# Kernel optimization log

Hardware: AMD Instinct MI355X
Metric: run time of the kernel (lower is better)

## Reference

```python
import jax, jax.numpy as jnp
import numpy as np

B, S, H, A = 64, 200, 256, 16
CAPS_LAYERS = 3
NEG = -1e9
LN_EPS = 1e-12


def _layernorm(x, g, b):
    mu = jnp.mean(x, axis=-1, keepdims=True)
    var = jnp.mean(jnp.square(x - mu), axis=-1, keepdims=True)
    return (x - mu) / jnp.sqrt(var + LN_EPS) * g + b


def setup_inputs() -> dict:
    key = jax.random.key(0)
    ks = jax.random.split(key, 10)
    s = 0.02  # initializer_range
    return {
        "item_emb": jax.random.normal(ks[0], (B, S, H), jnp.float32),
        "item_seq": jax.random.randint(ks[1], (B, S), 0, 50000),
        "time_seq": jax.random.randint(ks[2], (B, S, 2), 0, 14),
        "W_lin": s * jax.random.normal(ks[3], (H, H), jnp.float32),
        "b_lin": jnp.zeros((H,), jnp.float32),
        "aspect_embs": s * jax.random.normal(ks[4], (A, H), jnp.float32),
        "pos_emb": s * jax.random.normal(ks[5], (S, H), jnp.float32),
        "tdt_emb": s * jax.random.normal(ks[6], (14, H), jnp.float32),
        "tdn_emb": s * jax.random.normal(ks[7], (14, H), jnp.float32),
        "Wa1": s * jax.random.normal(ks[8], (H, H), jnp.float32),
        "ba1": jnp.zeros((H,), jnp.float32),
        "Wa2": s * jax.random.normal(ks[9], (H,), jnp.float32),
        "ba2": jnp.zeros((1,), jnp.float32),
        "ln_g": jnp.ones((H,), jnp.float32),
        "ln_b": jnp.zeros((H,), jnp.float32),
    }


def reference(item_emb, item_seq, time_seq, W_lin, b_lin, aspect_embs,
              pos_emb, tdt_emb, tdn_emb, Wa1, ba1, Wa2, ba2, ln_g, ln_b):
    b, s = item_emb.shape[0], item_emb.shape[1]
    pad = item_seq == 0  # [B,S]

    # ---- TimeAwareAttention (seq_output has a singleton neighbor dim in torch) ----
    td = tdt_emb[time_seq[:, :, 0]] + tdn_emb[time_seq[:, :, 1]]       # [B,S,H]
    tma_in = pos_emb[None, :s] + item_emb + td                          # [B,S,H]
    h = tma_in @ Wa1 + ba1
    h = jnp.where(h >= 0, h, 0.01 * h)                                  # LeakyReLU
    w = h @ Wa2 + ba2[0]                                                # [B,S]
    w = jnp.where(pad, NEG, w)
    tma = jax.nn.softmax(w, axis=-1)                                    # [B,S]

    # ---- gating (eval: clean gates) ----
    gates = jnp.einsum('bsh,ah->bsa', item_emb, aspect_embs)            # [B,S,A]
    idx = jnp.argmax(gates, axis=-1)                                    # topk k=1, [B,S]

    src = jnp.where(pad, 0.0, 1.0)
    counts = jnp.zeros((b, A), jnp.float32).at[jnp.arange(b)[:, None], idx].add(src)
    aspect_mask = counts == 0                                           # [B,A]

    # ---- item transform (dropout = identity in eval) ----
    moe = _layernorm(jnp.tanh(item_emb @ W_lin + b_lin) + item_emb, ln_g, ln_b)  # [B,S,H]

    # ---- capsule routing ----
    bij = gates
    cap = jnp.broadcast_to(aspect_embs[None], (b, A, H))
    for _ in range(CAPS_LAYERS):
        cij = jnp.where(aspect_mask[:, None, :], NEG, bij)
        cij = jax.nn.softmax(cij, axis=-1)
        cij = jnp.where(pad[:, :, None], 0.0, cij)                      # [B,S,A]
        cap = jnp.einsum('bsa,bsh,bs->bah', cij, moe, tma)              # [B,A,H]
        n2 = jnp.sum(jnp.square(cap), axis=-1, keepdims=True)
        cap = n2 / (1.0 + n2) / jnp.sqrt(n2 + 1e-9) * cap               # squash
        bij = bij + jnp.einsum('bsh,bah->bsa', moe, cap)

    # ---- gather activated interests / activation positions ----
    activated = cap[jnp.arange(b)[:, None], idx]                        # [B,S,H]
    seq_pos = jnp.where(pad, 0, jnp.arange(1, s + 1)[None, :]).astype(jnp.float32)
    act_mat = jnp.full((b, s, A), -1.0, jnp.float32)
    act_mat = act_mat.at[jnp.arange(b)[:, None], jnp.arange(s)[None, :], idx].set(seq_pos)
    act_mat = jnp.where(pad[:, :, None], -1.0, act_mat)
    max_pos = jnp.max(act_mat, axis=1)                                  # [B,A]
    aspects_item_idx = jnp.where(max_pos > -1.0, max_pos - 1.0, max_pos)

    gates_sm = jax.nn.softmax(gates, axis=-1)
    return (cap, gates_sm, aspect_mask, activated, aspects_item_idx, idx[:, :, None])
```

## Files before the change

kernel.cpp:

```cpp
#include <hip/hip_runtime.h>

#define B_ 64
#define S_ 200
#define H_ 256
#define A_ 16
#define M_ (B_*S_)
#define NEGV (-1000000000.0f)

typedef unsigned short ushortT;
typedef __attribute__((ext_vector_type(8))) short short8;
typedef __attribute__((ext_vector_type(4))) float f32x4;

__device__ __forceinline__ ushortT bf16u(float f) {
  unsigned int u = __builtin_bit_cast(unsigned int, f);
  unsigned int r = (u + 0x7fffu + ((u >> 16) & 1u)) >> 16;
  return (ushortT)r;
}
__device__ __forceinline__ float bf2f(ushortT u) {
  unsigned int v = ((unsigned int)u) << 16;
  return __builtin_bit_cast(float, v);
}

__global__ __launch_bounds__(256) void prep_kernel(
    const float* __restrict__ item, const int* __restrict__ iseq,
    const int* __restrict__ tseq, const float* __restrict__ Wa1,
    const float* __restrict__ W_lin, const float* __restrict__ asp,
    const float* __restrict__ pos, const float* __restrict__ tdt,
    const float* __restrict__ tdn,
    ushortT* __restrict__ itemB, ushortT* __restrict__ tmaB,
    ushortT* __restrict__ Wa1T, ushortT* __restrict__ WlinT,
    float* __restrict__ gates_raw, float* __restrict__ idxf)
{
  const int blk = blockIdx.x;
  const int t = threadIdx.x;

  if (blk >= 800) {
    __shared__ float T[64*65];
    int wsel = (blk - 800) >> 4;
    int tile = (blk - 800) & 15;
    const float* W = wsel ? W_lin : Wa1;
    ushortT* WT = wsel ? WlinT : Wa1T;
    int tr = (tile >> 2) * 64, tc = (tile & 3) * 64;
    #pragma unroll
    for (int p = 0; p < 16; ++p) {
      int r = p*4 + (t >> 6);
      int c = t & 63;
      T[c*65 + r] = W[(tr + r)*H_ + tc + c];
    }
    __syncthreads();
    #pragma unroll
    for (int p = 0; p < 16; ++p) {
      int n = p*4 + (t >> 6);
      int k = t & 63;
      WT[(tc + n)*H_ + tr + k] = bf16u(T[n*65 + k]);
    }
    return;
  }

  __shared__ float aspl[16*260];
  __shared__ float gL[16*20];
  __shared__ int sL[16], ttL[16], tnL[16];

  const int m0 = blk * 16;
  if (t < 16) {
    int m = m0 + t;
    sL[t]  = m % S_;
    ttL[t] = tseq[2*m];
    tnL[t] = tseq[2*m+1];
  }
  #pragma unroll
  for (int i = 0; i < 4; ++i) {
    int e = t + 256*i;
    int r = e >> 6, c = e & 63;
    *(float4*)&aspl[r*260 + 4*c] = *(const float4*)&asp[r*H_ + 4*c];
  }
  __syncthreads();

  #pragma unroll 4
  for (int r = 0; r < 16; ++r) {
    int m = m0 + r;
    float iv = item[(size_t)m*H_ + t];
    float tv = iv + pos[sL[r]*H_ + t] + tdt[ttL[r]*H_ + t] + tdn[tnL[r]*H_ + t];
    itemB[(size_t)m*H_ + t] = bf16u(iv);
    tmaB[(size_t)m*H_ + t]  = bf16u(tv);
  }

  {
    int r = t >> 4, a = t & 15;
    int m = m0 + r;
    float g = 0.f;
    #pragma unroll 4
    for (int k4 = 0; k4 < 64; ++k4) {
      float4 xv = *(const float4*)&item[(size_t)m*H_ + 4*k4];
      float4 av = *(const float4*)&aspl[a*260 + 4*k4];
      g += xv.x*av.x + xv.y*av.y + xv.z*av.z + xv.w*av.w;
    }
    gL[r*20 + a] = g;
  }
  __syncthreads();
  if (t < 64) {
    int r = t >> 2, q = t & 3;
    float4 gv;
    gv.x = gL[r*20 + 4*q + 0]; gv.y = gL[r*20 + 4*q + 1];
    gv.z = gL[r*20 + 4*q + 2]; gv.w = gL[r*20 + 4*q + 3];
    *(float4*)&gates_raw[(m0+r)*A_ + 4*q] = gv;
  }
  if (t < 16) {
    float best = gL[t*20]; int bi = 0;
    #pragma unroll
    for (int a = 1; a < 16; ++a) {
      float v = gL[t*20 + a];
      if (v > best) { best = v; bi = a; }
    }
    idxf[m0 + t] = (float)bi;
  }
}

__global__ __launch_bounds__(256) void gemm_kernel(
    const ushortT* __restrict__ tmaB, const ushortT* __restrict__ itemB,
    const ushortT* __restrict__ Wa1T, const ushortT* __restrict__ WlinT,
    const float* __restrict__ item, const int* __restrict__ iseq,
    const float* __restrict__ ba1, const float* __restrict__ Wa2,
    const float* __restrict__ ba2, const float* __restrict__ b_lin,
    const float* __restrict__ g_ln, const float* __restrict__ b_ln,
    float* __restrict__ w_out, ushortT* __restrict__ moe_outB)
{
  __shared__ ushortT Al[64*40];
  __shared__ ushortT Bl[256*40];

  const int g = blockIdx.y;
  const ushortT* __restrict__ Ap  = g ? itemB : tmaB;
  const ushortT* __restrict__ WTp = g ? WlinT : Wa1T;

  const int t = threadIdx.x;
  const int m0 = blockIdx.x * 64;
  const int lane = t & 63, w = t >> 6;
  const int col = lane & 15;
  const int rg  = lane >> 4;

  f32x4 acc[16];
  #pragma unroll
  for (int i = 0; i < 16; ++i) acc[i] = (f32x4){0.f,0.f,0.f,0.f};

  const int ar = t >> 2, akq = (t & 3) * 8;

  for (int k0 = 0; k0 < H_; k0 += 32) {
    __syncthreads();
    *(uint4*)&Al[ar*40 + akq] = *(const uint4*)&Ap[(size_t)(m0 + ar)*H_ + k0 + akq];
    #pragma unroll
    for (int i = 0; i < 4; ++i) {
      int n = i*64 + ar;
      *(uint4*)&Bl[n*40 + akq] = *(const uint4*)&WTp[(size_t)n*H_ + k0 + akq];
    }
    __syncthreads();
    short8 af = *(const short8*)&Al[(w*16 + col)*40 + rg*8];
    #pragma unroll
    for (int q = 0; q < 16; ++q) {
      short8 bf = *(const short8*)&Bl[(q*16 + col)*40 + rg*8];
      acc[q] = __builtin_amdgcn_mfma_f32_16x16x32_bf16(af, bf, acc[q], 0, 0, 0);
    }
  }

  if (g == 0) {
    float bav[16], wav[16];
    #pragma unroll
    for (int q = 0; q < 16; ++q) {
      int n = q*16 + col;
      bav[q] = ba1[n]; wav[q] = Wa2[n];
    }
    float bb2 = ba2[0];
    #pragma unroll
    for (int j = 0; j < 4; ++j) {
      float p = 0.f;
      #pragma unroll
      for (int q = 0; q < 16; ++q) {
        float h = acc[q][j] + bav[q];
        h = (h >= 0.f) ? h : 0.01f*h;
        p += h * wav[q];
      }
      #pragma unroll
      for (int mk = 1; mk < 16; mk <<= 1) p += __shfl_xor(p, mk);
      if (col == 0) {
        int m = m0 + w*16 + rg*4 + j;
        w_out[m] = (iseq[m] == 0) ? NEGV : (p + bb2);
      }
    }
  } else {
    float blv[16], glv[16], bbv[16];
    #pragma unroll
    for (int q = 0; q < 16; ++q) {
      int n = q*16 + col;
      blv[q] = b_lin[n]; glv[q] = g_ln[n]; bbv[q] = b_ln[n];
    }
    #pragma unroll
    for (int j = 0; j < 4; ++j) {
      int m = m0 + w*16 + rg*4 + j;
      float v[16];
      float s1 = 0.f, s2 = 0.f;
      #pragma unroll
      for (int q = 0; q < 16; ++q) {
        float iv = item[(size_t)m*H_ + q*16 + col];
        float vv = tanhf(acc[q][j] + blv[q]) + iv;
        v[q] = vv; s1 += vv; s2 += vv*vv;
      }
      #pragma unroll
      for (int mk = 1; mk < 16; mk <<= 1) {
        s1 += __shfl_xor(s1, mk);
        s2 += __shfl_xor(s2, mk);
      }
      float mu  = s1 * (1.0f/H_);
      float var = s2 * (1.0f/H_) - mu*mu;
      float rs  = 1.0f / sqrtf(fmaxf(var, 0.f) + 1e-12f);
      #pragma unroll
      for (int q = 0; q < 16; ++q)
        moe_outB[(size_t)m*H_ + q*16 + col] = bf16u((v[q] - mu)*rs*glv[q] + bbv[q]);
    }
  }
}

__device__ __forceinline__ float blk_max(float v, float* red) {
  #pragma unroll
  for (int mk = 32; mk; mk >>= 1) v = fmaxf(v, __shfl_xor(v, mk));
  int t = threadIdx.x;
  if ((t & 63) == 0) red[t >> 6] = v;
  __syncthreads();
  if (t < 64) {
    float x = (t < 16) ? red[t] : -3.0e38f;
    #pragma unroll
    for (int mk = 8; mk; mk >>= 1) x = fmaxf(x, __shfl_xor(x, mk));
    if (t == 0) red[0] = x;
  }
  __syncthreads();
  float r = red[0];
  __syncthreads();
  return r;
}

__device__ __forceinline__ float blk_sum(float v, float* red) {
  #pragma unroll
  for (int mk = 32; mk; mk >>= 1) v += __shfl_xor(v, mk);
  int t = threadIdx.x;
  if ((t & 63) == 0) red[t >> 6] = v;
  __syncthreads();
  if (t < 64) {
    float x = (t < 16) ? red[t] : 0.f;
    #pragma unroll
    for (int mk = 8; mk; mk >>= 1) x += __shfl_xor(x, mk);
    if (t == 0) red[0] = x;
  }
  __syncthreads();
  float r = red[0];
  __syncthreads();
  return r;
}

#define WGSTR 232
#define CBSTR 260
#define CLSTR 252

__global__ __launch_bounds__(1024) void phaseC_kernel(
    const int* __restrict__ iseq, const float* __restrict__ w_in,
    const ushortT* __restrict__ moeB, const float* __restrict__ idxf,
    float* __restrict__ gates_rs,
    float* __restrict__ cap_out,
    float* __restrict__ mask_out,
    float* __restrict__ aidx_out,
    float* __restrict__ act_out)
{
  __shared__ ushortT moeTr[57344];
  __shared__ ushortT wgtT[16*WGSTR];
  __shared__ ushortT capB[16*CBSTR];
  __shared__ float bij[4032];
  __shared__ float n2p[16*17];
  __shared__ float n2s[16];
  __shared__ float tmaL[S_];
  __shared__ float red[16];
  __shared__ float maskf[A_];
  __shared__ int counts[A_], maxpos[A_];
  __shared__ int idxl[S_];
  __shared__ int padl[S_];

  const int t = threadIdx.x;
  const int b = blockIdx.x;
  const int base = b * S_;
  const int lane = t & 63, w = t >> 6;
  const int la = lane & 15, lg = lane >> 4;

  #pragma unroll
  for (int u = 0; u < 4; ++u) {
    int e = t + 1024*u;
    if (e < 3584) {
      int ht = e & 15, s = e >> 4;
      int ks = s >> 5, s4l = (s >> 2) & 7, sr = s & 3;
      int bp = (s4l & 1) ? 4 + (s4l >> 1) : (s4l >> 1);
      int li = ((ht*7 + ks)*8 + bp)*64 + sr*16;
      if (s < S_) {
        const ushortT* gp = &moeB[((size_t)(base + s))*H_ + ht*16];
        *(uint4*)&moeTr[li]     = *(const uint4*)gp;
        *(uint4*)&moeTr[li + 8] = *(const uint4*)(gp + 8);
      } else {
        uint4 z = {0,0,0,0};
        *(uint4*)&moeTr[li] = z; *(uint4*)&moeTr[li + 8] = z;
      }
    }
  }
  if (t < 512) {
    int a = t >> 5, s = 200 + (t & 31);
    wgtT[a*WGSTR + s] = 0;
  }

  if (t < A_) { counts[t] = 0; maxpos[t] = -1; }
  float wv = -3.0e38f;
  if (t < S_) {
    int s = t;
    padl[s] = (iseq[base+s] == 0) ? 1 : 0;
    idxl[s] = (int)idxf[base+s];
    wv = w_in[base+s];
    #pragma unroll
    for (int q = 0; q < 4; ++q)
      *(float4*)&bij[s*20 + 4*q] = *(const float4*)&gates_rs[(base+s)*A_ + 4*q];
  }
  __syncthreads();

  if (t < S_ && !padl[t]) {
    atomicAdd(&counts[idxl[t]], 1);
    atomicMax(&maxpos[idxl[t]], t + 1);
  }
  if (t < S_) {
    int s = t;
    float row[16]; float mx = -3.0e38f;
    #pragma unroll
    for (int a = 0; a < 16; ++a) { row[a] = bij[s*20+a]; mx = fmaxf(mx, row[a]); }
    float sm = 0.f;
    #pragma unroll
    for (int a = 0; a < 16; ++a) { row[a] = expf(row[a] - mx); sm += row[a]; }
    float inv = 1.f / sm;
    #pragma unroll
    for (int q = 0; q < 4; ++q) {
      float4 o; o.x=row[4*q]*inv; o.y=row[4*q+1]*inv; o.z=row[4*q+2]*inv; o.w=row[4*q+3]*inv;
      *(float4*)&gates_rs[(base+s)*A_ + 4*q] = o;
    }
  }
  float mxw = blk_max(wv, red);
  float ev = (t < S_) ? expf(wv - mxw) : 0.f;
  float sw = blk_sum(ev, red);
  if (t < S_) tmaL[t] = ev / sw;
  __syncthreads();
  if (t < A_) {
    int c = counts[t];
    float mkv = (c == 0) ? 1.f : 0.f;
    maskf[t] = mkv;
    mask_out[b*A_ + t] = mkv;
    int mp = maxpos[t];
    aidx_out[b*A_ + t] = (mp > 0) ? (float)(mp - 1) : -1.f;
  }
  __syncthreads();

  for (int iter = 0; iter < 3; ++iter) {
    if (t < S_) {
      int s = t;
      float row[16]; float mx = -3.0e38f;
      #pragma unroll
      for (int a = 0; a < 16; ++a) {
        float v = bij[s*20+a];
        v = (maskf[a] > 0.5f) ? NEGV : v;
        row[a] = v; mx = fmaxf(mx, v);
      }
      float sm = 0.f;
      #pragma unroll
      for (int a = 0; a < 16; ++a) { row[a] = expf(row[a] - mx); sm += row[a]; }
      float sc = (padl[s] ? 0.f : tmaL[s]) / sm;
      #pragma unroll
      for (int a = 0; a < 16; ++a) wgtT[a*WGSTR + s] = bf16u(row[a]*sc);
    }
    __syncthreads();

    f32x4 acc = (f32x4){0.f,0.f,0.f,0.f};
    {
      unsigned vA = (unsigned)(w*7168 + lane*8);
      #pragma unroll
      for (int ks = 0; ks < 7; ++ks) {
        unsigned vAk = vA + (unsigned)(ks*1024);
        long long r0, r1;
        asm volatile(
          "ds_read_b64_tr_b16 %0, %2\n\t"
          "ds_read_b64_tr_b16 %1, %2 offset:512\n\t"
          "s_waitcnt lgkmcnt(0)"
          : "=&v"(r0), "=&v"(r1) : "v"(vAk) : "memory");
        __builtin_amdgcn_sched_barrier(0);
        union { short8 v; long long q[2]; } uu;
        uu.q[0] = r0; uu.q[1] = r1;
        short8 bf = *(const short8*)&wgtT[la*WGSTR + ks*32 + lg*8];
        acc = __builtin_amdgcn_mfma_f32_16x16x32_bf16(uu.v, bf, acc, 0, 0, 0);
      }
    }
    {
      float n2 = acc[0]*acc[0] + acc[1]*acc[1] + acc[2]*acc[2] + acc[3]*acc[3];
      n2 += __shfl_xor(n2, 16);
      n2 += __shfl_xor(n2, 32);
      if (lane < 16) n2p[w*17 + lane] = n2;
    }
    __syncthreads();
    if (t < 16) {
      float sv = 0.f;
      #pragma unroll
      for (int w2 = 0; w2 < 16; ++w2) sv += n2p[w2*17 + t];
      n2s[t] = sv / (1.f + sv) / sqrtf(sv + 1e-9f);
    }
    __syncthreads();
    {
      float sc = n2s[la];
      if (iter < 2) {
        #pragma unroll
        for (int r = 0; r < 4; ++r)
          capB[la*CBSTR + w*16 + lg*4 + r] = bf16u(acc[r]*sc);
      } else {
        float* capl = bij;
        #pragma unroll
        for (int r = 0; r < 4; ++r)
          capl[la*CLSTR + w*16 + lg*4 + r] = acc[r]*sc;
      }
    }
    __syncthreads();

    if (iter < 2) {
      if (w < 13) {
        int sR = w*16 + la;
        int ksS = sR >> 5, s4l = (sR >> 2) & 7, sr = sR & 3;
        int bp = (s4l & 1) ? 4 + (s4l >> 1) : (s4l >> 1);
        int laneA = ksS*512 + bp*64 + sr*16 + (lg & 1)*8 + (lg >> 1)*3584;
        f32x4 accS = (f32x4){0.f,0.f,0.f,0.f};
        #pragma unroll
        for (int k4 = 0; k4 < 8; ++k4) {
          short8 am = *(const short8*)&moeTr[laneA + k4*7168];
          short8 bc = *(const short8*)&capB[la*CBSTR + k4*32 + lg*8];
          accS = __builtin_amdgcn_mfma_f32_16x16x32_bf16(am, bc, accS, 0, 0, 0);
        }
        int sW = w*16 + lg*4;
        #pragma unroll
        for (int r = 0; r < 4; ++r)
          if (sW + r < S_) bij[(sW + r)*20 + la] += accS[r];
      }
      __syncthreads();
    }
  }

  {
    const float* capl = bij;
    #pragma unroll
    for (int q = 0; q < 4; ++q) {
      int e = t + 1024*q;
      int a = e >> 8, h = e & 255;
      cap_out[((size_t)b*A_ + a)*H_ + h] = capl[a*CLSTR + h];
    }
    int h4 = t & 63;
    for (int s = t >> 6; s < S_; s += 16) {
      float4 v = *(const float4*)&capl[idxl[s]*CLSTR + 4*h4];
      *(float4*)&act_out[((size_t)base + s)*H_ + 4*h4] = v;
    }
  }
}

extern "C" void kernel_launch(void* const* d_in, const int* in_sizes, int n_in,
                              void* d_out, int out_size, void* d_ws, size_t ws_size,
                              hipStream_t stream) {
  (void)in_sizes; (void)n_in; (void)out_size; (void)ws_size;
  const float* item  = (const float*)d_in[0];
  const int*   iseq  = (const int*)d_in[1];
  const int*   tseq  = (const int*)d_in[2];
  const float* W_lin = (const float*)d_in[3];
  const float* b_lin = (const float*)d_in[4];
  const float* asp   = (const float*)d_in[5];
  const float* pos   = (const float*)d_in[6];
  const float* tdt   = (const float*)d_in[7];
  const float* tdn   = (const float*)d_in[8];
  const float* Wa1   = (const float*)d_in[9];
  const float* ba1   = (const float*)d_in[10];
  const float* Wa2   = (const float*)d_in[11];
  const float* ba2   = (const float*)d_in[12];
  const float* g_ln  = (const float*)d_in[13];
  const float* b_ln  = (const float*)d_in[14];

  float* out    = (float*)d_out;
  float* cap_o  = out;
  float* gate_o = out + 262144;
  float* mask_o = out + 466944;
  float* act_o  = out + 467968;
  float* aidx_o = out + 3744768;
  float* idx_o  = out + 3745792;

  ushortT* moeB  = (ushortT*)d_ws;
  ushortT* Wa1T  = (ushortT*)((char*)d_ws + 6553600);
  ushortT* WlinT = Wa1T + 65536;
  float*   w_ws  = (float*)((char*)d_ws + 6553600 + 262144);

  ushortT* itemB = (ushortT*)act_o;
  ushortT* tmaB  = itemB + (size_t)M_*H_;

  prep_kernel<<<832, 256, 0, stream>>>(item, iseq, tseq, Wa1, W_lin, asp,
      pos, tdt, tdn, itemB, tmaB, Wa1T, WlinT, gate_o, idx_o);
  gemm_kernel<<<dim3(M_/64, 2), 256, 0, stream>>>(tmaB, itemB, Wa1T, WlinT,
      item, iseq, ba1, Wa2, ba2, b_lin, g_ln, b_ln, w_ws, moeB);
  phaseC_kernel<<<B_, 1024, 0, stream>>>(iseq, w_ws, moeB, idx_o,
      gate_o, cap_o, mask_o, aidx_o, act_o);
}
```

Baseline: 60.99 us.

## Fuse bf16 input staging into GEMM and merge both GEMMs per block

```diff
diff --git a/kernel.cpp b/kernel.cpp
--- a/kernel.cpp
+++ b/kernel.cpp
@@ -22,12 +22,8 @@
 }
 
 __global__ __launch_bounds__(256) void prep_kernel(
-    const float* __restrict__ item, const int* __restrict__ iseq,
-    const int* __restrict__ tseq, const float* __restrict__ Wa1,
+    const float* __restrict__ item, const float* __restrict__ Wa1,
     const float* __restrict__ W_lin, const float* __restrict__ asp,
-    const float* __restrict__ pos, const float* __restrict__ tdt,
-    const float* __restrict__ tdn,
-    ushortT* __restrict__ itemB, ushortT* __restrict__ tmaB,
     ushortT* __restrict__ Wa1T, ushortT* __restrict__ WlinT,
     float* __restrict__ gates_raw, float* __restrict__ idxf)
 {
@@ -59,15 +55,8 @@
 
   __shared__ float aspl[16*260];
   __shared__ float gL[16*20];
-  __shared__ int sL[16], ttL[16], tnL[16];
 
   const int m0 = blk * 16;
-  if (t < 16) {
-    int m = m0 + t;
-    sL[t]  = m % S_;
-    ttL[t] = tseq[2*m];
-    tnL[t] = tseq[2*m+1];
-  }
   #pragma unroll
   for (int i = 0; i < 4; ++i) {
     int e = t + 256*i;
@@ -75,15 +64,6 @@
     *(float4*)&aspl[r*260 + 4*c] = *(const float4*)&asp[r*H_ + 4*c];
   }
   __syncthreads();
-
-  #pragma unroll 4
-  for (int r = 0; r < 16; ++r) {
-    int m = m0 + r;
-    float iv = item[(size_t)m*H_ + t];
-    float tv = iv + pos[sL[r]*H_ + t] + tdt[ttL[r]*H_ + t] + tdn[tnL[r]*H_ + t];
-    itemB[(size_t)m*H_ + t] = bf16u(iv);
-    tmaB[(size_t)m*H_ + t]  = bf16u(tv);
-  }
 
   {
     int r = t >> 4, a = t & 15;
@@ -116,47 +96,75 @@
   }
 }
 
-__global__ __launch_bounds__(256) void gemm_kernel(
-    const ushortT* __restrict__ tmaB, const ushortT* __restrict__ itemB,
+__global__ __launch_bounds__(512, 2) void gemm_kernel(
+    const float* __restrict__ item, const int* __restrict__ iseq,
+    const int* __restrict__ tseq, const float* __restrict__ pos,
+    const float* __restrict__ tdt, const float* __restrict__ tdn,
     const ushortT* __restrict__ Wa1T, const ushortT* __restrict__ WlinT,
-    const float* __restrict__ item, const int* __restrict__ iseq,
     const float* __restrict__ ba1, const float* __restrict__ Wa2,
     const float* __restrict__ ba2, const float* __restrict__ b_lin,
     const float* __restrict__ g_ln, const float* __restrict__ b_ln,
     float* __restrict__ w_out, ushortT* __restrict__ moe_outB)
 {
-  __shared__ ushortT Al[64*40];
-  __shared__ ushortT Bl[256*40];
-
-  const int g = blockIdx.y;
-  const ushortT* __restrict__ Ap  = g ? itemB : tmaB;
-  const ushortT* __restrict__ WTp = g ? WlinT : Wa1T;
+  __shared__ ushortT Atma[64*40];
+  __shared__ ushortT Aitm[64*40];
+  __shared__ ushortT B0l[256*40];
+  __shared__ ushortT B1l[256*40];
+  __shared__ int sL[64], ttL[64], tnL[64];
 
   const int t = threadIdx.x;
   const int m0 = blockIdx.x * 64;
   const int lane = t & 63, w = t >> 6;
+  const int g = w >> 2, wl = w & 3;
   const int col = lane & 15;
   const int rg  = lane >> 4;
+
+  if (t < 64) {
+    int m = m0 + t;
+    sL[t]  = m % S_;
+    ttL[t] = tseq[2*m];
+    tnL[t] = tseq[2*m+1];
+  }
 
   f32x4 acc[16];
   #pragma unroll
   for (int i = 0; i < 16; ++i) acc[i] = (f32x4){0.f,0.f,0.f,0.f};
 
-  const int ar = t >> 2, akq = (t & 3) * 8;
+  const int ar = t >> 3, kq = (t & 7) * 4;
+  const int nr = t >> 1, kh = (t & 1) * 16;
+
+  __syncthreads();
 
   for (int k0 = 0; k0 < H_; k0 += 32) {
-    __syncthreads();
-    *(uint4*)&Al[ar*40 + akq] = *(const uint4*)&Ap[(size_t)(m0 + ar)*H_ + k0 + akq];
-    #pragma unroll
-    for (int i = 0; i < 4; ++i) {
-      int n = i*64 + ar;
-      *(uint4*)&Bl[n*40 + akq] = *(const uint4*)&WTp[(size_t)n*H_ + k0 + akq];
-    }
-    __syncthreads();
-    short8 af = *(const short8*)&Al[(w*16 + col)*40 + rg*8];
+    float4 iv = *(const float4*)&item[(size_t)(m0 + ar)*H_ + k0 + kq];
+    float4 pv = *(const float4*)&pos[sL[ar]*H_ + k0 + kq];
+    float4 tv = *(const float4*)&tdt[ttL[ar]*H_ + k0 + kq];
+    float4 nv = *(const float4*)&tdn[tnL[ar]*H_ + k0 + kq];
+    union { ushortT u[4]; uint2 v; } ci, ct;
+    ci.u[0] = bf16u(iv.x); ci.u[1] = bf16u(iv.y);
+    ci.u[2] = bf16u(iv.z); ci.u[3] = bf16u(iv.w);
+    ct.u[0] = bf16u(iv.x + pv.x + tv.x + nv.x);
+    ct.u[1] = bf16u(iv.y + pv.y + tv.y + nv.y);
+    ct.u[2] = bf16u(iv.z + pv.z + tv.z + nv.z);
+    ct.u[3] = bf16u(iv.w + pv.w + tv.w + nv.w);
+    uint4 b0a = *(const uint4*)&Wa1T[(size_t)nr*H_ + k0 + kh];
+    uint4 b0b = *(const uint4*)&Wa1T[(size_t)nr*H_ + k0 + kh + 8];
+    uint4 b1a = *(const uint4*)&WlinT[(size_t)nr*H_ + k0 + kh];
+    uint4 b1b = *(const uint4*)&WlinT[(size_t)nr*H_ + k0 + kh + 8];
+    __syncthreads();
+    *(uint2*)&Aitm[ar*40 + kq] = ci.v;
+    *(uint2*)&Atma[ar*40 + kq] = ct.v;
+    *(uint4*)&B0l[nr*40 + kh]     = b0a;
+    *(uint4*)&B0l[nr*40 + kh + 8] = b0b;
+    *(uint4*)&B1l[nr*40 + kh]     = b1a;
+    *(uint4*)&B1l[nr*40 + kh + 8] = b1b;
+    __syncthreads();
+    const ushortT* Ab = g ? Aitm : Atma;
+    const ushortT* Bb = g ? B1l : B0l;
+    short8 af = *(const short8*)&Ab[(wl*16 + col)*40 + rg*8];
     #pragma unroll
     for (int q = 0; q < 16; ++q) {
-      short8 bf = *(const short8*)&Bl[(q*16 + col)*40 + rg*8];
+      short8 bf = *(const short8*)&Bb[(q*16 + col)*40 + rg*8];
       acc[q] = __builtin_amdgcn_mfma_f32_16x16x32_bf16(af, bf, acc[q], 0, 0, 0);
     }
   }
@@ -181,7 +189,7 @@
       #pragma unroll
       for (int mk = 1; mk < 16; mk <<= 1) p += __shfl_xor(p, mk);
       if (col == 0) {
-        int m = m0 + w*16 + rg*4 + j;
+        int m = m0 + wl*16 + rg*4 + j;
         w_out[m] = (iseq[m] == 0) ? NEGV : (p + bb2);
       }
     }
@@ -194,13 +202,13 @@
     }
     #pragma unroll
     for (int j = 0; j < 4; ++j) {
-      int m = m0 + w*16 + rg*4 + j;
+      int m = m0 + wl*16 + rg*4 + j;
       float v[16];
       float s1 = 0.f, s2 = 0.f;
       #pragma unroll
       for (int q = 0; q < 16; ++q) {
-        float iv = item[(size_t)m*H_ + q*16 + col];
-        float vv = tanhf(acc[q][j] + blv[q]) + iv;
+        float ivv = item[(size_t)m*H_ + q*16 + col];
+        float vv = tanhf(acc[q][j] + blv[q]) + ivv;
         v[q] = vv; s1 += vv; s2 += vv*vv;
       }
       #pragma unroll
@@ -494,13 +502,10 @@
   ushortT* WlinT = Wa1T + 65536;
   float*   w_ws  = (float*)((char*)d_ws + 6553600 + 262144);
 
-  ushortT* itemB = (ushortT*)act_o;
-  ushortT* tmaB  = itemB + (size_t)M_*H_;
-
-  prep_kernel<<<832, 256, 0, stream>>>(item, iseq, tseq, Wa1, W_lin, asp,
-      pos, tdt, tdn, itemB, tmaB, Wa1T, WlinT, gate_o, idx_o);
-  gemm_kernel<<<dim3(M_/64, 2), 256, 0, stream>>>(tmaB, itemB, Wa1T, WlinT,
-      item, iseq, ba1, Wa2, ba2, b_lin, g_ln, b_ln, w_ws, moeB);
+  prep_kernel<<<832, 256, 0, stream>>>(item, Wa1, W_lin, asp,
+      Wa1T, WlinT, gate_o, idx_o);
+  gemm_kernel<<<200, 512, 0, stream>>>(item, iseq, tseq, pos, tdt, tdn,
+      Wa1T, WlinT, ba1, Wa2, ba2, b_lin, g_ln, b_ln, w_ws, moeB);
   phaseC_kernel<<<B_, 1024, 0, stream>>>(iseq, w_ws, moeB, idx_o,
       gate_o, cap_o, mask_o, aidx_o, act_o);
 }
```

New measurement: 59.53 us. 2.4% less time.
